# Optimization experiments

Hardware: AMD Instinct MI355X
Metric: run time of the kernel (lower is better)

The kernel has to match this reference:

```python
import jax, jax.numpy as jnp
import numpy as np

SEQ, BATCH, FEATURES, D_MODEL, N_LAYER = 2048, 64, 64, 256, 2


def setup_inputs() -> dict:
    key = jax.random.key(0)
    ks = jax.random.split(key, 10)
    s = 0.05
    H = D_MODEL
    return {
        "input_ids": jax.random.normal(ks[0], (SEQ, BATCH, FEATURES), jnp.float32),
        "enc_w": jax.random.normal(ks[1], (H, FEATURES), jnp.float32) * s,
        "enc_b": jax.random.normal(ks[2], (H,), jnp.float32) * s,
        # PyTorch LSTM layout: gates stacked as [i, f, g, o] along first axis
        "w_ih": jax.random.normal(ks[3], (N_LAYER, 4 * H, H), jnp.float32) * s,
        "w_hh": jax.random.normal(ks[4], (N_LAYER, 4 * H, H), jnp.float32) * s,
        "b_ih": jax.random.normal(ks[5], (N_LAYER, 4 * H), jnp.float32) * s,
        "b_hh": jax.random.normal(ks[6], (N_LAYER, 4 * H), jnp.float32) * s,
        "dec_w": jax.random.normal(ks[7], (FEATURES, H), jnp.float32) * s,
        "dec_b": jax.random.normal(ks[8], (FEATURES,), jnp.float32) * s,
    }


def _lstm_layer(x, w_ih_l, w_hh_l, b_ih_l, b_hh_l):
    # x: (S, B, H). Precompute input projections for all timesteps at once.
    S, B, H = x.shape
    xg = jnp.einsum('sbh,gh->sbg', x, w_ih_l) + b_ih_l + b_hh_l  # (S, B, 4H)

    def step(carry, xg_t):
        h, c = carry
        gates = xg_t + h @ w_hh_l.T  # (B, 4H)
        i, f, g, o = jnp.split(gates, 4, axis=-1)
        i = jax.nn.sigmoid(i)
        f = jax.nn.sigmoid(f)
        g = jnp.tanh(g)
        o = jax.nn.sigmoid(o)
        c = f * c + i * g
        h = o * jnp.tanh(c)
        return (h, c), h

    h0 = jnp.zeros((B, H), x.dtype)
    c0 = jnp.zeros((B, H), x.dtype)
    _, ys = jax.lax.scan(step, (h0, c0), xg)
    return ys  # (S, B, H)


def reference(input_ids, enc_w, enc_b, w_ih, w_hh, b_ih, b_hh, dec_w, dec_b):
    x = input_ids @ enc_w.T + enc_b  # (S, B, H)
    n_layer = w_ih.shape[0]
    for l in range(n_layer):
        x = _lstm_layer(x, w_ih[l], w_hh[l], b_ih[l], b_hh[l])
    return x @ dec_w.T + dec_b  # (S, B, features)
```

## Files before the change

### kernel.cpp

```cpp
#include <hip/hip_runtime.h>


typedef unsigned short u16;
typedef unsigned long long u64;
typedef __attribute__((ext_vector_type(8))) short short8;
typedef __attribute__((ext_vector_type(4))) float f32x4;

#define SEQ  2048
#define CS   128
#define NCH  (SEQ / CS)
#define CN   (CS * 64)
#define SLOT 16384
#define HXBYTES ((size_t)(CS + 1) * SLOT * 2)
#define SENT64 0x7F7F7F7F7F7F7F7FULL

__device__ __forceinline__ u16 f2bf(float f) {
  unsigned u = __float_as_uint(f);
  unsigned r = u + 0x7fffu + ((u >> 16) & 1u);
  return (u16)(r >> 16);
}
__device__ __forceinline__ float bf2f(u16 h) {
  return __uint_as_float(((unsigned)h) << 16);
}
__device__ __forceinline__ float sigf(float x) {
  return __builtin_amdgcn_rcpf(1.f + __expf(-x));
}
__device__ __forceinline__ float tanhf_fast(float x) {
  return 1.f - 2.f * __builtin_amdgcn_rcpf(1.f + __expf(2.f * x));
}

__device__ __forceinline__ u64 aload(const u16* p) {
  return __hip_atomic_load((const u64*)p, __ATOMIC_RELAXED, __HIP_MEMORY_SCOPE_AGENT);
}
__device__ __forceinline__ void astore(u16* p, u64 v) {
  __hip_atomic_store((u64*)p, v, __ATOMIC_RELAXED, __HIP_MEMORY_SCOPE_AGENT);
}

__device__ __forceinline__ int rowp_to_orig(int rowp) {
  int p = rowp >> 8, T = (rowp >> 4) & 15, u = rowp & 15;
  int g = u & 3;
  int j = ((T >> 2) << 4) + ((u >> 2) << 2) + (T & 3);
  return g * 256 + p * 64 + j;
}

#define PREP_TOTAL (16384 + 65536 + 1024 + 1024 + 524288 + 262144 + 32768)

__global__ void prep_kernel(const float* __restrict__ enc_w, const float* __restrict__ enc_b,
                            const float* __restrict__ w_ih, const float* __restrict__ w_hh,
                            const float* __restrict__ b_ih, const float* __restrict__ b_hh,
                            const float* __restrict__ dec_w,
                            u16* __restrict__ WDEC, u16* __restrict__ CW,
                            float* __restrict__ CB, float* __restrict__ B1P,
                            u16* __restrict__ WHHP, u16* __restrict__ WIH1P,
                            u16* __restrict__ HX0, u16* __restrict__ HX1)
{
  size_t idx = (size_t)blockIdx.x * 256 + threadIdx.x;
  if (idx < 16384) { WDEC[idx] = f2bf(dec_w[idx]); return; }
  idx -= 16384;
  if (idx < 65536) {
    int rowp = (int)(idx >> 6), f = (int)(idx & 63);
    int r = rowp_to_orig(rowp);
    float a = 0.f;
    for (int k = 0; k < 256; ++k) a += w_ih[r * 256 + k] * enc_w[k * 64 + f];
    CW[idx] = f2bf(a);
    return;
  }
  idx -= 65536;
  if (idx < 1024) {
    int r = rowp_to_orig((int)idx);
    float a = b_ih[r] + b_hh[r];
    for (int k = 0; k < 256; ++k) a += w_ih[r * 256 + k] * enc_b[k];
    CB[idx] = a;
    return;
  }
  idx -= 1024;
  if (idx < 1024) {
    int r = rowp_to_orig((int)idx);
    B1P[idx] = b_ih[1024 + r] + b_hh[1024 + r];
    return;
  }
  idx -= 1024;
  if (idx < 524288) {
    int l = (int)(idx >> 18);
    int rem = (int)(idx & 262143);
    int e = rem & 7, lane = (rem >> 3) & 63, kc = (rem >> 9) & 7;
    int t = (rem >> 12) & 3, wv = (rem >> 14) & 3, pp = (rem >> 16) & 3;
    int u = lane & 15, qd = lane >> 4;
    int g = u & 3;
    int j = wv * 16 + ((u >> 2) << 2) + t;
    int r = g * 256 + pp * 64 + j;
    int k = kc * 32 + qd * 8 + e;
    WHHP[idx] = f2bf(w_hh[(size_t)l * 262144 + (size_t)r * 256 + k]);
    return;
  }
  idx -= 524288;
  if (idx < 262144) {
    int rem = (int)idx;
    int e = rem & 7, lane = (rem >> 3) & 63, kc = (rem >> 9) & 7;
    int t = (rem >> 12) & 3, wv = (rem >> 14) & 3, pp = (rem >> 16) & 3;
    int u = lane & 15, qd = lane >> 4;
    int g = u & 3;
    int j = wv * 16 + ((u >> 2) << 2) + t;
    int r = g * 256 + pp * 64 + j;
    int k = kc * 32 + qd * 8 + e;
    WIH1P[idx] = f2bf(w_ih[262144 + (size_t)r * 256 + k]);
    return;
  }
  idx -= 262144;
  if (idx < 32768) {
    if (idx < 16384) HX0[idx] = 0;
    else             HX1[idx - 16384] = 0;
  }
}

template<int KTILES, int OUTBF, int BMODE, int AF32>
__global__ __launch_bounds__(256, 1) void gemm_bt(
    const void* __restrict__ Av, const u16* __restrict__ B, void* __restrict__ Cv,
    const float* __restrict__ bias, size_t ldc)
{
  constexpr int K = KTILES * 64;
  __shared__ __align__(16) u16 Asl[64 * 72];
  __shared__ __align__(16) u16 Bsl[64 * 72];
  const int tid = threadIdx.x;
  const int w = tid >> 6, lane = tid & 63, lm = lane & 15, quad = lane >> 4;
  const size_t m0 = (size_t)blockIdx.y * 64, n0 = (size_t)blockIdx.x * 64;

  f32x4 acc[4];
#pragma unroll
  for (int nt = 0; nt < 4; ++nt) { f32x4 z = {0.f, 0.f, 0.f, 0.f}; acc[nt] = z; }

  for (int kb = 0; kb < KTILES; ++kb) {
    if (AF32) {
      const float* Af = (const float*)Av;
#pragma unroll
      for (int c = 0; c < 4; ++c) {
        int idx = c * 256 + tid;
        int row = idx >> 4, k4 = idx & 15;
        float4 v = *(const float4*)(Af + (m0 + row) * (size_t)K + kb * 64 + k4 * 4);
        u64 pv = (u64)f2bf(v.x) | ((u64)f2bf(v.y) << 16) |
                 ((u64)f2bf(v.z) << 32) | ((u64)f2bf(v.w) << 48);
        *(u64*)(&Asl[row * 72 + k4 * 4]) = pv;
      }
    } else {
      const u16* Ab = (const u16*)Av;
#pragma unroll
      for (int c = 0; c < 2; ++c) {
        int idx = c * 256 + tid;
        int row = idx >> 3, k8 = idx & 7;
        *(uint4*)(&Asl[row * 72 + k8 * 8]) =
            *(const uint4*)(Ab + (m0 + row) * (size_t)K + kb * 64 + k8 * 8);
      }
    }
#pragma unroll
    for (int c = 0; c < 2; ++c) {
      int idx = c * 256 + tid;
      int row = idx >> 3, k8 = idx & 7;
      *(uint4*)(&Bsl[row * 72 + k8 * 8]) =
          *(const uint4*)(B + (n0 + row) * (size_t)K + kb * 64 + k8 * 8);
    }
    __syncthreads();
#pragma unroll
    for (int kc = 0; kc < 2; ++kc) {
      short8 a = *(const short8*)(&Asl[(w * 16 + lm) * 72 + kc * 32 + quad * 8]);
#pragma unroll
      for (int nt = 0; nt < 4; ++nt) {
        short8 b = *(const short8*)(&Bsl[(nt * 16 + lm) * 72 + kc * 32 + quad * 8]);
        acc[nt] = __builtin_amdgcn_mfma_f32_16x16x32_bf16(a, b, acc[nt], 0, 0, 0);
      }
    }
    __syncthreads();
  }
#pragma unroll
  for (int nt = 0; nt < 4; ++nt) {
    size_t n = n0 + nt * 16 + lm;
    float bn = (BMODE == 1) ? bias[n] : 0.f;
#pragma unroll
    for (int r = 0; r < 4; ++r) {
      size_t m = m0 + w * 16 + quad * 4 + r;
      float v = acc[nt][r] + ((BMODE == 2) ? bias[m] : bn);
      if (OUTBF) ((u16*)Cv)[m * ldc + n] = f2bf(v);
      else       ((float*)Cv)[m * ldc + n] = v;
    }
  }
}

__device__ __forceinline__ void gather32(const u16* __restrict__ src,
                                         u16* __restrict__ dst,
                                         int tid, int n2, bool skip, int p)
{
  const int j4 = tid & 63;
  const bool need = !(skip && ((j4 >> 4) == p));
  u64 v[8];
#pragma unroll
  for (int i = 0; i < 8; ++i) {
    int lb = i * 4 + (tid >> 6);
    v[i] = need ? aload(src + ((size_t)(n2 * 32 + lb) * 256 + j4 * 4)) : 0;
  }
  for (;;) {
    bool bad = false;
#pragma unroll
    for (int i = 0; i < 8; ++i) bad |= (v[i] == SENT64);
    if (!bad) break;
#pragma unroll
    for (int i = 0; i < 8; ++i)
      if (v[i] == SENT64) {
        int lb = i * 4 + (tid >> 6);
        v[i] = aload(src + ((size_t)(n2 * 32 + lb) * 256 + j4 * 4));
      }
  }
  if (need) {
#pragma unroll
    for (int i = 0; i < 8; ++i) {
      int lb = i * 4 + (tid >> 6);
      *(u64*)(dst + lb * 264 + j4 * 4) = v[i];
    }
  }
}

__global__ __launch_bounds__(256, 1) void lstm_fused(
    const u16* __restrict__ xg0, u16* __restrict__ x2,
    const u16* __restrict__ whhp, const u16* __restrict__ wih1p,
    const float* __restrict__ b1p,
    u16* __restrict__ hx0, u16* __restrict__ hx1,
    float* __restrict__ cstb, int base)
{
  __shared__ __align__(16) u16 Hl[2][2][32 * 264];
  const int tid = threadIdx.x;
  const int role = blockIdx.x;
  const int layer = role >> 3, p = role & 3, n2 = (role >> 2) & 1;
  const int lane = tid & 63, w = tid >> 6, lm = lane & 15, quad = lane >> 4;

  short8 wfh[4][8], wfi[4][8];
  {
    const u16* wp = whhp + (size_t)((layer * 4 + p) * 4 + w) * 16384 + lane * 8;
#pragma unroll
    for (int t = 0; t < 4; ++t)
#pragma unroll
      for (int kc = 0; kc < 8; ++kc)
        wfh[t][kc] = *(const short8*)(wp + (t * 8 + kc) * 512);
  }
  f32x4 bias_f[4];
  if (layer) {
    const u16* wp = wih1p + (size_t)(p * 4 + w) * 16384 + lane * 8;
#pragma unroll
    for (int t = 0; t < 4; ++t)
#pragma unroll
      for (int kc = 0; kc < 8; ++kc)
        wfi[t][kc] = *(const short8*)(wp + (t * 8 + kc) * 512);
#pragma unroll
    for (int t = 0; t < 4; ++t)
      bias_f[t] = *(const f32x4*)(b1p + p * 256 + (w * 4 + t) * 16 + quad * 4);
  }

  float* cp = cstb + (size_t)(((layer * 4 + p) * 2 + n2) * 256 + tid) * 8;
  float cst[4][2];
  if (base) {
#pragma unroll
    for (int t = 0; t < 4; ++t) { cst[t][0] = cp[t * 2]; cst[t][1] = cp[t * 2 + 1]; }
  } else {
#pragma unroll
    for (int t = 0; t < 4; ++t) { cst[t][0] = 0.f; cst[t][1] = 0.f; }
  }

  const int jcol = p * 64 + w * 16 + quad * 4;
  u16* myhx = layer ? hx1 : hx0;
  u64 hprev[2] = {0, 0};

  for (int s = 1; s <= CS; ++s) {
    const int cur = s & 1;
    const bool own = (s > 1);
    u64 xv[4][2];
    if (layer == 0) {
#pragma unroll
      for (int t = 0; t < 4; ++t)
#pragma unroll
        for (int nt = 0; nt < 2; ++nt)
          xv[t][nt] = *(const u64*)(xg0 +
              ((size_t)(s - 1) * 64 + n2 * 32 + nt * 16 + lm) * 1024 +
              p * 256 + (w * 4 + t) * 16 + quad * 4);
    }
    if (layer == 0) {
      gather32(hx0 + (size_t)(s - 1) * SLOT, &Hl[cur][0][0], tid, n2, own, p);
      if (own) {
#pragma unroll
        for (int nt = 0; nt < 2; ++nt)
          *(u64*)(&Hl[cur][0][(nt * 16 + lm) * 264 + jcol]) = hprev[nt];
      }
    } else {
      gather32(hx1 + (size_t)(s - 1) * SLOT, &Hl[cur][1][0], tid, n2, own, p);
      if (own) {
#pragma unroll
        for (int nt = 0; nt < 2; ++nt)
          *(u64*)(&Hl[cur][1][(nt * 16 + lm) * 264 + jcol]) = hprev[nt];
      }
      gather32(hx0 + (size_t)s * SLOT, &Hl[cur][0][0], tid, n2, false, p);
    }
    __builtin_amdgcn_sched_barrier(0);
    asm volatile("s_waitcnt lgkmcnt(0)" ::: "memory");
    __builtin_amdgcn_s_barrier();
    __builtin_amdgcn_sched_barrier(0);

    f32x4 acc[4][2];
    if (layer == 0) {
#pragma unroll
      for (int t = 0; t < 4; ++t)
#pragma unroll
        for (int nt = 0; nt < 2; ++nt) {
          u64 v = xv[t][nt];
          f32x4 tt = { bf2f((u16)v), bf2f((u16)(v >> 16)),
                       bf2f((u16)(v >> 32)), bf2f((u16)(v >> 48)) };
          acc[t][nt] = tt;
        }
    } else {
#pragma unroll
      for (int t = 0; t < 4; ++t)
#pragma unroll
        for (int nt = 0; nt < 2; ++nt) acc[t][nt] = bias_f[t];
    }
    if (layer == 0) {
#pragma unroll
      for (int kc = 0; kc < 8; ++kc) {
        short8 b0[2];
#pragma unroll
        for (int nt = 0; nt < 2; ++nt)
          b0[nt] = *(const short8*)(&Hl[cur][0][(nt * 16 + lm) * 264 + kc * 32 + quad * 8]);
#pragma unroll
        for (int t = 0; t < 4; ++t)
#pragma unroll
          for (int nt = 0; nt < 2; ++nt)
            acc[t][nt] = __builtin_amdgcn_mfma_f32_16x16x32_bf16(
                wfh[t][kc], b0[nt], acc[t][nt], 0, 0, 0);
      }
    } else {
#pragma unroll
      for (int kc = 0; kc < 8; ++kc) {
        short8 b0[2];
#pragma unroll
        for (int nt = 0; nt < 2; ++nt)
          b0[nt] = *(const short8*)(&Hl[cur][0][(nt * 16 + lm) * 264 + kc * 32 + quad * 8]);
#pragma unroll
        for (int t = 0; t < 4; ++t)
#pragma unroll
          for (int nt = 0; nt < 2; ++nt)
            acc[t][nt] = __builtin_amdgcn_mfma_f32_16x16x32_bf16(
                wfi[t][kc], b0[nt], acc[t][nt], 0, 0, 0);
      }
#pragma unroll
      for (int kc = 0; kc < 8; ++kc) {
        short8 b1[2];
#pragma unroll
        for (int nt = 0; nt < 2; ++nt)
          b1[nt] = *(const short8*)(&Hl[cur][1][(nt * 16 + lm) * 264 + kc * 32 + quad * 8]);
#pragma unroll
        for (int t = 0; t < 4; ++t)
#pragma unroll
          for (int nt = 0; nt < 2; ++nt)
            acc[t][nt] = __builtin_amdgcn_mfma_f32_16x16x32_bf16(
                wfh[t][kc], b1[nt], acc[t][nt], 0, 0, 0);
      }
    }
    u16* hd = myhx + (size_t)s * SLOT;
#pragma unroll
    for (int nt = 0; nt < 2; ++nt) {
      u64 h = 0;
#pragma unroll
      for (int t = 0; t < 4; ++t) {
        float iv = sigf(acc[t][nt][0]);
        float fv = sigf(acc[t][nt][1]);
        float gv = tanhf_fast(acc[t][nt][2]);
        float ov = sigf(acc[t][nt][3]);
        float cv = fv * cst[t][nt] + iv * gv;
        cst[t][nt] = cv;
        h |= (u64)f2bf(ov * tanhf_fast(cv)) << (16 * t);
      }
      const int b = n2 * 32 + nt * 16 + lm;
      astore(hd + (size_t)b * 256 + jcol, h);
      if (s == CS) astore(myhx + (size_t)b * 256 + jcol, h);
      if (layer) *(u64*)(x2 + ((size_t)(s - 1) * 64 + b) * 256 + jcol) = h;
      hprev[nt] = h;
    }
  }
#pragma unroll
  for (int t = 0; t < 4; ++t) { cp[t * 2] = cst[t][0]; cp[t * 2 + 1] = cst[t][1]; }
}

extern "C" void kernel_launch(void* const* d_in, const int* in_sizes, int n_in,
                              void* d_out, int out_size, void* d_ws, size_t ws_size,
                              hipStream_t stream)
{
  const float* in0   = (const float*)d_in[0];
  const float* enc_w = (const float*)d_in[1];
  const float* enc_b = (const float*)d_in[2];
  const float* w_ih  = (const float*)d_in[3];
  const float* w_hh  = (const float*)d_in[4];
  const float* b_ih  = (const float*)d_in[5];
  const float* b_hh  = (const float*)d_in[6];
  const float* dec_w = (const float*)d_in[7];
  const float* dec_b = (const float*)d_in[8];

  char* ws = (char*)d_ws;
  u16*   XG    = (u16*)(ws);
  u16*   X2    = (u16*)(ws + 16777216);
  u16*   WHHP  = (u16*)(ws + 20971520);
  u16*   WIH1P = (u16*)(ws + 22020096);
  u16*   CW    = (u16*)(ws + 22544384);
  u16*   WDEC  = (u16*)(ws + 22675456);
  float* CB    = (float*)(ws + 22708224);
  float* B1P   = (float*)(ws + 22712320);
  u16*   HX0   = (u16*)(ws + 22716416);
  u16*   HX1   = (u16*)(ws + 26943488);
  float* CST   = (float*)(ws + 31170560);

  if (ws_size < 31301632) return;

  hipMemsetAsync(HX0, 0x7F, HXBYTES, stream);
  hipMemsetAsync(HX1, 0x7F, HXBYTES, stream);

  prep_kernel<<<dim3((PREP_TOTAL + 255) / 256), 256, 0, stream>>>(
      enc_w, enc_b, w_ih, w_hh, b_ih, b_hh, dec_w,
      WDEC, CW, CB, B1P, WHHP, WIH1P, HX0, HX1);

  for (int c = 0; c < NCH; ++c) {
    const float* inc = in0 + (size_t)c * CN * 64;
    float* outc = (float*)d_out + (size_t)c * CN * 64;
    gemm_bt<1, 1, 1, 1><<<dim3(16, CN / 64), 256, 0, stream>>>(inc, CW, XG, CB, 1024);
    lstm_fused<<<dim3(16), 256, 0, stream>>>(XG, X2, WHHP, WIH1P, B1P,
                                             HX0, HX1, CST, c * CS);
    if (c + 1 < NCH) {
      hipMemsetAsync((char*)HX0 + SLOT * 2, 0x7F, HXBYTES - SLOT * 2, stream);
      hipMemsetAsync((char*)HX1 + SLOT * 2, 0x7F, HXBYTES - SLOT * 2, stream);
    }
    gemm_bt<4, 0, 1, 0><<<dim3(1, CN / 64), 256, 0, stream>>>(X2, WDEC, (void*)outc, dec_b, 64);
  }

  (void)in_sizes; (void)n_in; (void)out_size;
}
```

Before: 8.274 ms.

## Pin LSTM blocks to two XCDs and use sc0 spin loads for h exchange

```diff
diff --git a/kernel.cpp b/kernel.cpp
--- a/kernel.cpp
+++ b/kernel.cpp
@@ -34,6 +34,24 @@
 }
 __device__ __forceinline__ void astore(u16* p, u64 v) {
   __hip_atomic_store((u64*)p, v, __ATOMIC_RELAXED, __HIP_MEMORY_SCOPE_AGENT);
+}
+__device__ __forceinline__ void st_plain(u16* p, u64 v) {
+  asm volatile("global_store_dwordx2 %0, %1, off" :: "v"(p), "v"(v));
+}
+__device__ __forceinline__ void ld8_sc0(const u16* a0, u64 v[8]) {
+  asm volatile(
+      "global_load_dwordx2 %0, %8, off sc0\n\t"
+      "global_load_dwordx2 %1, %8, off offset:2048 sc0\n\t"
+      "global_load_dwordx2 %2, %9, off sc0\n\t"
+      "global_load_dwordx2 %3, %9, off offset:2048 sc0\n\t"
+      "global_load_dwordx2 %4, %10, off sc0\n\t"
+      "global_load_dwordx2 %5, %10, off offset:2048 sc0\n\t"
+      "global_load_dwordx2 %6, %11, off sc0\n\t"
+      "global_load_dwordx2 %7, %11, off offset:2048 sc0\n\t"
+      "s_waitcnt vmcnt(0)"
+      : "=&v"(v[0]), "=&v"(v[1]), "=&v"(v[2]), "=&v"(v[3]),
+        "=&v"(v[4]), "=&v"(v[5]), "=&v"(v[6]), "=&v"(v[7])
+      : "v"(a0), "v"(a0 + 2048), "v"(a0 + 4096), "v"(a0 + 6144));
 }
 
 __device__ __forceinline__ int rowp_to_orig(int rowp) {
@@ -189,32 +207,27 @@
                                          int tid, int n2, bool skip, int p)
 {
   const int j4 = tid & 63;
+  const int tw = tid >> 6;
   const bool need = !(skip && ((j4 >> 4) == p));
+  if (!need) return;
+  const u16* a0 = src + ((size_t)(n2 * 32 + tw) * 256 + j4 * 4);
   u64 v[8];
-#pragma unroll
-  for (int i = 0; i < 8; ++i) {
-    int lb = i * 4 + (tid >> 6);
-    v[i] = need ? aload(src + ((size_t)(n2 * 32 + lb) * 256 + j4 * 4)) : 0;
-  }
-  for (;;) {
+  ld8_sc0(a0, v);
+  for (int spin = 1;; ++spin) {
     bool bad = false;
 #pragma unroll
     for (int i = 0; i < 8; ++i) bad |= (v[i] == SENT64);
     if (!bad) break;
-#pragma unroll
-    for (int i = 0; i < 8; ++i)
-      if (v[i] == SENT64) {
-        int lb = i * 4 + (tid >> 6);
-        v[i] = aload(src + ((size_t)(n2 * 32 + lb) * 256 + j4 * 4));
-      }
-  }
-  if (need) {
-#pragma unroll
-    for (int i = 0; i < 8; ++i) {
-      int lb = i * 4 + (tid >> 6);
-      *(u64*)(dst + lb * 264 + j4 * 4) = v[i];
-    }
-  }
+    if (spin & 7) {
+      ld8_sc0(a0, v);
+    } else {
+#pragma unroll
+      for (int i = 0; i < 8; ++i) v[i] = aload(a0 + (size_t)i * 1024);
+    }
+  }
+#pragma unroll
+  for (int i = 0; i < 8; ++i)
+    *(u64*)(dst + (i * 4 + tw) * 264 + j4 * 4) = v[i];
 }
 
 __global__ __launch_bounds__(256, 1) void lstm_fused(
@@ -224,10 +237,14 @@
     u16* __restrict__ hx0, u16* __restrict__ hx1,
     float* __restrict__ cstb, int base)
 {
+  const int bid = blockIdx.x;
+  const int xcd = bid & 7, slot = bid >> 3;
+  if (xcd >= 2) return;
+  const int n2 = xcd;
+  const int layer = slot >> 2, p = slot & 3;
+
   __shared__ __align__(16) u16 Hl[2][2][32 * 264];
   const int tid = threadIdx.x;
-  const int role = blockIdx.x;
-  const int layer = role >> 3, p = role & 3, n2 = (role >> 2) & 1;
   const int lane = tid & 63, w = tid >> 6, lm = lane & 15, quad = lane >> 4;
 
   short8 wfh[4][8], wfi[4][8];
@@ -275,9 +292,9 @@
       for (int t = 0; t < 4; ++t)
 #pragma unroll
         for (int nt = 0; nt < 2; ++nt)
-          xv[t][nt] = *(const u64*)(xg0 +
+          xv[t][nt] = __builtin_nontemporal_load((const u64*)(xg0 +
               ((size_t)(s - 1) * 64 + n2 * 32 + nt * 16 + lm) * 1024 +
-              p * 256 + (w * 4 + t) * 16 + quad * 4);
+              p * 256 + (w * 4 + t) * 16 + quad * 4));
     }
     if (layer == 0) {
       gather32(hx0 + (size_t)(s - 1) * SLOT, &Hl[cur][0][0], tid, n2, own, p);
@@ -374,9 +391,16 @@
         h |= (u64)f2bf(ov * tanhf_fast(cv)) << (16 * t);
       }
       const int b = n2 * 32 + nt * 16 + lm;
-      astore(hd + (size_t)b * 256 + jcol, h);
-      if (s == CS) astore(myhx + (size_t)b * 256 + jcol, h);
-      if (layer) *(u64*)(x2 + ((size_t)(s - 1) * 64 + b) * 256 + jcol) = h;
+      u16* pd = hd + (size_t)b * 256 + jcol;
+      st_plain(pd, h);
+      astore(pd, h);
+      if (s == CS) {
+        u16* ps = myhx + (size_t)b * 256 + jcol;
+        st_plain(ps, h);
+        astore(ps, h);
+      }
+      if (layer)
+        __builtin_nontemporal_store(h, (u64*)(x2 + ((size_t)(s - 1) * 64 + b) * 256 + jcol));
       hprev[nt] = h;
     }
   }
@@ -424,7 +448,7 @@
     const float* inc = in0 + (size_t)c * CN * 64;
     float* outc = (float*)d_out + (size_t)c * CN * 64;
     gemm_bt<1, 1, 1, 1><<<dim3(16, CN / 64), 256, 0, stream>>>(inc, CW, XG, CB, 1024);
-    lstm_fused<<<dim3(16), 256, 0, stream>>>(XG, X2, WHHP, WIH1P, B1P,
+    lstm_fused<<<dim3(64), 256, 0, stream>>>(XG, X2, WHHP, WIH1P, B1P,
                                              HX0, HX1, CST, c * CS);
     if (c + 1 < NCH) {
       hipMemsetAsync((char*)HX0 + SLOT * 2, 0x7F, HXBYTES - SLOT * 2, stream);
```

Measured after the change: 16.94 ms. 2.05x slower.

## Overlap layer-0 hidden-state fetch with layer-1 recurrent MFMA and batch loads in asm

Applied to the files above, without the earlier changes.

```diff
diff --git a/kernel.cpp b/kernel.cpp
--- a/kernel.cpp
+++ b/kernel.cpp
@@ -34,6 +34,38 @@
 }
 __device__ __forceinline__ void astore(u16* p, u64 v) {
   __hip_atomic_store((u64*)p, v, __ATOMIC_RELAXED, __HIP_MEMORY_SCOPE_AGENT);
+}
+
+__device__ __forceinline__ void ld8_issue(const u16* a0, u64 v[8]) {
+  asm volatile(
+      "global_load_dwordx2 %0, %8, off sc0 sc1\n\t"
+      "global_load_dwordx2 %1, %8, off offset:2048 sc0 sc1\n\t"
+      "global_load_dwordx2 %2, %9, off sc0 sc1\n\t"
+      "global_load_dwordx2 %3, %9, off offset:2048 sc0 sc1\n\t"
+      "global_load_dwordx2 %4, %10, off sc0 sc1\n\t"
+      "global_load_dwordx2 %5, %10, off offset:2048 sc0 sc1\n\t"
+      "global_load_dwordx2 %6, %11, off sc0 sc1\n\t"
+      "global_load_dwordx2 %7, %11, off offset:2048 sc0 sc1"
+      : "=&v"(v[0]), "=&v"(v[1]), "=&v"(v[2]), "=&v"(v[3]),
+        "=&v"(v[4]), "=&v"(v[5]), "=&v"(v[6]), "=&v"(v[7])
+      : "v"(a0), "v"(a0 + 2048), "v"(a0 + 4096), "v"(a0 + 6144)
+      : "memory");
+}
+__device__ __forceinline__ void vmwait8(u64 v[8]) {
+  asm volatile("s_waitcnt vmcnt(0)"
+      : "+v"(v[0]), "+v"(v[1]), "+v"(v[2]), "+v"(v[3]),
+        "+v"(v[4]), "+v"(v[5]), "+v"(v[6]), "+v"(v[7]) :: "memory");
+}
+__device__ __forceinline__ void ld8_agent(const u16* a0, u64 v[8]) {
+  ld8_issue(a0, v);
+  vmwait8(v);
+}
+
+__device__ __forceinline__ void wg_barrier() {
+  __builtin_amdgcn_sched_barrier(0);
+  asm volatile("s_waitcnt lgkmcnt(0)" ::: "memory");
+  __builtin_amdgcn_s_barrier();
+  __builtin_amdgcn_sched_barrier(0);
 }
 
 __device__ __forceinline__ int rowp_to_orig(int rowp) {
@@ -189,32 +221,22 @@
                                          int tid, int n2, bool skip, int p)
 {
   const int j4 = tid & 63;
+  const int tw = tid >> 6;
   const bool need = !(skip && ((j4 >> 4) == p));
+  if (!need) return;
+  const u16* a0 = src + ((size_t)(n2 * 32 + tw) * 256 + j4 * 4);
   u64 v[8];
-#pragma unroll
-  for (int i = 0; i < 8; ++i) {
-    int lb = i * 4 + (tid >> 6);
-    v[i] = need ? aload(src + ((size_t)(n2 * 32 + lb) * 256 + j4 * 4)) : 0;
-  }
+  ld8_agent(a0, v);
   for (;;) {
     bool bad = false;
 #pragma unroll
     for (int i = 0; i < 8; ++i) bad |= (v[i] == SENT64);
     if (!bad) break;
-#pragma unroll
-    for (int i = 0; i < 8; ++i)
-      if (v[i] == SENT64) {
-        int lb = i * 4 + (tid >> 6);
-        v[i] = aload(src + ((size_t)(n2 * 32 + lb) * 256 + j4 * 4));
-      }
-  }
-  if (need) {
-#pragma unroll
-    for (int i = 0; i < 8; ++i) {
-      int lb = i * 4 + (tid >> 6);
-      *(u64*)(dst + lb * 264 + j4 * 4) = v[i];
-    }
-  }
+    ld8_agent(a0, v);
+  }
+#pragma unroll
+  for (int i = 0; i < 8; ++i)
+    *(u64*)(dst + (i * 4 + tw) * 264 + j4 * 4) = v[i];
 }
 
 __global__ __launch_bounds__(256, 1) void lstm_fused(
@@ -229,6 +251,7 @@
   const int role = blockIdx.x;
   const int layer = role >> 3, p = role & 3, n2 = (role >> 2) & 1;
   const int lane = tid & 63, w = tid >> 6, lm = lane & 15, quad = lane >> 4;
+  const int j4 = tid & 63, tw = tid >> 6;
 
   short8 wfh[4][8], wfi[4][8];
   {
@@ -269,8 +292,10 @@
   for (int s = 1; s <= CS; ++s) {
     const int cur = s & 1;
     const bool own = (s > 1);
-    u64 xv[4][2];
+    f32x4 acc[4][2];
+
     if (layer == 0) {
+      u64 xv[4][2];
 #pragma unroll
       for (int t = 0; t < 4; ++t)
 #pragma unroll
@@ -278,30 +303,13 @@
           xv[t][nt] = *(const u64*)(xg0 +
               ((size_t)(s - 1) * 64 + n2 * 32 + nt * 16 + lm) * 1024 +
               p * 256 + (w * 4 + t) * 16 + quad * 4);
-    }
-    if (layer == 0) {
       gather32(hx0 + (size_t)(s - 1) * SLOT, &Hl[cur][0][0], tid, n2, own, p);
       if (own) {
 #pragma unroll
         for (int nt = 0; nt < 2; ++nt)
           *(u64*)(&Hl[cur][0][(nt * 16 + lm) * 264 + jcol]) = hprev[nt];
       }
-    } else {
-      gather32(hx1 + (size_t)(s - 1) * SLOT, &Hl[cur][1][0], tid, n2, own, p);
-      if (own) {
-#pragma unroll
-        for (int nt = 0; nt < 2; ++nt)
-          *(u64*)(&Hl[cur][1][(nt * 16 + lm) * 264 + jcol]) = hprev[nt];
-      }
-      gather32(hx0 + (size_t)s * SLOT, &Hl[cur][0][0], tid, n2, false, p);
-    }
-    __builtin_amdgcn_sched_barrier(0);
-    asm volatile("s_waitcnt lgkmcnt(0)" ::: "memory");
-    __builtin_amdgcn_s_barrier();
-    __builtin_amdgcn_sched_barrier(0);
-
-    f32x4 acc[4][2];
-    if (layer == 0) {
+      wg_barrier();
 #pragma unroll
       for (int t = 0; t < 4; ++t)
 #pragma unroll
@@ -311,13 +319,6 @@
                        bf2f((u16)(v >> 32)), bf2f((u16)(v >> 48)) };
           acc[t][nt] = tt;
         }
-    } else {
-#pragma unroll
-      for (int t = 0; t < 4; ++t)
-#pragma unroll
-        for (int nt = 0; nt < 2; ++nt) acc[t][nt] = bias_f[t];
-    }
-    if (layer == 0) {
 #pragma unroll
       for (int kc = 0; kc < 8; ++kc) {
         short8 b0[2];
@@ -332,6 +333,46 @@
                 wfh[t][kc], b0[nt], acc[t][nt], 0, 0, 0);
       }
     } else {
+      gather32(hx1 + (size_t)(s - 1) * SLOT, &Hl[cur][1][0], tid, n2, own, p);
+      if (own) {
+#pragma unroll
+        for (int nt = 0; nt < 2; ++nt)
+          *(u64*)(&Hl[cur][1][(nt * 16 + lm) * 264 + jcol]) = hprev[nt];
+      }
+      const u16* ah = hx0 + (size_t)s * SLOT +
+                      ((size_t)(n2 * 32 + tw) * 256 + j4 * 4);
+      u64 vh[8];
+      ld8_issue(ah, vh);
+      wg_barrier();
+#pragma unroll
+      for (int t = 0; t < 4; ++t)
+#pragma unroll
+        for (int nt = 0; nt < 2; ++nt) acc[t][nt] = bias_f[t];
+#pragma unroll
+      for (int kc = 0; kc < 8; ++kc) {
+        short8 b1[2];
+#pragma unroll
+        for (int nt = 0; nt < 2; ++nt)
+          b1[nt] = *(const short8*)(&Hl[cur][1][(nt * 16 + lm) * 264 + kc * 32 + quad * 8]);
+#pragma unroll
+        for (int t = 0; t < 4; ++t)
+#pragma unroll
+          for (int nt = 0; nt < 2; ++nt)
+            acc[t][nt] = __builtin_amdgcn_mfma_f32_16x16x32_bf16(
+                wfh[t][kc], b1[nt], acc[t][nt], 0, 0, 0);
+      }
+      vmwait8(vh);
+      for (;;) {
+        bool bad = false;
+#pragma unroll
+        for (int i = 0; i < 8; ++i) bad |= (vh[i] == SENT64);
+        if (!bad) break;
+        ld8_agent(ah, vh);
+      }
+#pragma unroll
+      for (int i = 0; i < 8; ++i)
+        *(u64*)(&Hl[cur][0][(i * 4 + tw) * 264 + j4 * 4]) = vh[i];
+      wg_barrier();
 #pragma unroll
       for (int kc = 0; kc < 8; ++kc) {
         short8 b0[2];
@@ -345,20 +386,8 @@
             acc[t][nt] = __builtin_amdgcn_mfma_f32_16x16x32_bf16(
                 wfi[t][kc], b0[nt], acc[t][nt], 0, 0, 0);
       }
-#pragma unroll
-      for (int kc = 0; kc < 8; ++kc) {
-        short8 b1[2];
-#pragma unroll
-        for (int nt = 0; nt < 2; ++nt)
-          b1[nt] = *(const short8*)(&Hl[cur][1][(nt * 16 + lm) * 264 + kc * 32 + quad * 8]);
-#pragma unroll
-        for (int t = 0; t < 4; ++t)
-#pragma unroll
-          for (int nt = 0; nt < 2; ++nt)
-            acc[t][nt] = __builtin_amdgcn_mfma_f32_16x16x32_bf16(
-                wfh[t][kc], b1[nt], acc[t][nt], 0, 0, 0);
-      }
-    }
+    }
+
     u16* hd = myhx + (size_t)s * SLOT;
 #pragma unroll
     for (int nt = 0; nt < 2; ++nt) {
```

After: 7.554 ms. -8.7%, faster.
